# Performance work log

Hardware: AMD Instinct MI355X
Metric: run time of the kernel (lower is better)

Reference implementation:

```python
import jax, jax.numpy as jnp
import numpy as np

NHEAD = 8
STRIP = 7  # strip_width (horizontal strips, is_vertical=False)


def setup_inputs() -> dict:
    key = jax.random.key(0)
    k0, k1, k2 = jax.random.split(key, 3)
    B, H, W, C = 2, 112, 112, 256
    x = jax.random.normal(k0, (B, H * W, C), dtype=jnp.float32)
    # torch nn.Linear weights: (out_features, in_features)
    qkv_w = jax.random.normal(k1, (3 * C, C), dtype=jnp.float32) * 0.02
    proj_w = jax.random.normal(k2, (C, C), dtype=jnp.float32) * 0.02
    proj_b = jnp.zeros((C,), dtype=jnp.float32)
    return {"x": x, "qkv_w": qkv_w, "proj_w": proj_w, "proj_b": proj_b,
            "H_feat": 112, "W_feat": 112}


def reference(x, qkv_w, proj_w, proj_b, H_feat, W_feat):
    B, N, C = x.shape
    hd = C // NHEAD
    scale = hd ** -0.5
    n_strips = H_feat // STRIP
    L = STRIP * W_feat  # tokens per horizontal strip
    # window_partition with window (STRIP, W_feat): nwW==1, so a pure reshape
    xs = x.reshape(B * n_strips, L, C)
    # qkv projection (Linear: y = x @ W^T), then split q/k/v and heads
    qkv = jnp.einsum('bnc,dc->bnd', xs, qkv_w)
    qkv = qkv.reshape(B * n_strips, L, 3, NHEAD, hd)
    q, k, v = jnp.moveaxis(qkv, 2, 0)  # each (Bw, L, H, hd)
    attn = jnp.einsum('bnhd,bmhd->bhnm', q * scale, k)
    attn = jax.nn.softmax(attn, axis=-1)
    out = jnp.einsum('bhnm,bmhd->bnhd', attn, v).reshape(B * n_strips, L, C)
    out = jnp.einsum('bnc,dc->bnd', out, proj_w) + proj_b
    # window_reverse is again a pure reshape for horizontal strips
    return out.reshape(B, N, C)
```

## Files before the change

kernel.cpp:

```cpp
#include <hip/hip_runtime.h>
#include <hip/hip_bf16.h>

#define M_ROWS 25088
#define CDIM   256
#define QKVD   768
#define LWIN   784
#define NWINH  256

typedef __attribute__((ext_vector_type(8))) short short8v;
typedef __attribute__((ext_vector_type(4))) float floatx4;

#define CEQ 0.2550660106245232f

static __device__ __forceinline__ unsigned short f2bf(float f) {
    unsigned int x = __float_as_uint(f);
    x += 0x7fffu + ((x >> 16) & 1u);
    return (unsigned short)(x >> 16);
}
static __device__ __forceinline__ unsigned int cvt_pk_bf16(float a, float b) {
    unsigned int r;
    asm("v_cvt_pk_bf16_f32 %0, %1, %2" : "=v"(r) : "v"(a), "v"(b));
    return r;
}
static __device__ __forceinline__ void gld_lds16(const unsigned short* g,
                                                 unsigned short* l) {
    __builtin_amdgcn_global_load_lds(
        (const __attribute__((address_space(1))) unsigned int*)g,
        (__attribute__((address_space(3))) unsigned int*)l, 16, 0, 0);
}

#define N8_TOTAL ((M_ROWS * CDIM + QKVD * CDIM + CDIM * CDIM) / 8)

__global__ __launch_bounds__(256) void k_f2bf3(
    const float* __restrict__ s0,
    const float* __restrict__ s1,
    const float* __restrict__ s2,
    unsigned short* __restrict__ d0,
    unsigned short* __restrict__ d1,
    unsigned short* __restrict__ d2)
{
    const int n80 = (M_ROWS * CDIM) / 8;
    const int n81 = (QKVD * CDIM) / 8;
    for (int i = blockIdx.x * 256 + threadIdx.x; i < N8_TOTAL;
         i += gridDim.x * 256) {
        const float4* s4;
        uint4* d4;
        int j = i;
        if (j < n80)            { s4 = (const float4*)s0; d4 = (uint4*)d0; }
        else if ((j -= n80) < n81) { s4 = (const float4*)s1; d4 = (uint4*)d1; }
        else                    { j -= n81; s4 = (const float4*)s2; d4 = (uint4*)d2; }
        float4 a = s4[2 * j], b = s4[2 * j + 1];
        uint4 o;
        o.x = cvt_pk_bf16(a.x, a.y);
        o.y = cvt_pk_bf16(a.z, a.w);
        o.z = cvt_pk_bf16(b.x, b.y);
        o.w = cvt_pk_bf16(b.z, b.w);
        d4[j] = o;
    }
}

template <typename OUT_T, bool BIAS, bool SCALEQ>
__global__ __launch_bounds__(256, 2) void k_gemm_mfma(
    const unsigned short* __restrict__ A,
    const unsigned short* __restrict__ B,
    const float* __restrict__ bias,
    OUT_T* __restrict__ Y, int N)
{
    __shared__ __attribute__((aligned(16))) unsigned short As[128 * 64];
    __shared__ __attribute__((aligned(16))) unsigned short Bs[128 * 64];
    const int t = threadIdx.x;
    const int lane = t & 63, wv = t >> 6;
    const int lq = lane & 15, g = lane >> 4;
    const int wm = wv >> 1, wn = wv & 1;
    const int R0 = blockIdx.y * 128, C0 = blockIdx.x * 128;
    const int lrow = t >> 3, lch = (t & 7) * 8;

    floatx4 acc[4][4];
#pragma unroll
    for (int i = 0; i < 4; ++i)
#pragma unroll
        for (int j = 0; j < 4; ++j) acc[i][j] = (floatx4){0.f, 0.f, 0.f, 0.f};

    for (int kc = 0; kc < 256; kc += 64) {
#pragma unroll
        for (int i = 0; i < 4; ++i) {
            gld_lds16(A + (size_t)(R0 + i * 32 + lrow) * 256 + kc + lch,
                      As + (i * 32 + wv * 8) * 64);
            gld_lds16(B + (size_t)(C0 + i * 32 + lrow) * 256 + kc + lch,
                      Bs + (i * 32 + wv * 8) * 64);
        }
        __syncthreads();
#pragma unroll
        for (int kk = 0; kk < 64; kk += 32) {
            short8v af[4], bf[4];
#pragma unroll
            for (int mi = 0; mi < 4; ++mi)
                af[mi] = *(const short8v*)(As + (wm * 64 + mi * 16 + lq) * 64 +
                                           kk + g * 8);
#pragma unroll
            for (int ni = 0; ni < 4; ++ni)
                bf[ni] = *(const short8v*)(Bs + (wn * 64 + ni * 16 + lq) * 64 +
                                           kk + g * 8);
#pragma unroll
            for (int mi = 0; mi < 4; ++mi)
#pragma unroll
                for (int ni = 0; ni < 4; ++ni)
                    acc[mi][ni] = __builtin_amdgcn_mfma_f32_16x16x32_bf16(
                        af[mi], bf[ni], acc[mi][ni], 0, 0, 0);
        }
        __syncthreads();
    }

#pragma unroll
    for (int mi = 0; mi < 4; ++mi) {
        const size_t rb = (size_t)R0 + wm * 64 + mi * 16 + g * 4;
#pragma unroll
        for (int ni = 0; ni < 4; ++ni) {
            const int col = C0 + wn * 64 + ni * 16 + lq;
            float bv = 0.f;
            if constexpr (BIAS) bv = bias[col];
#pragma unroll
            for (int r = 0; r < 4; ++r) {
                float val = acc[mi][ni][r];
                if constexpr (SCALEQ) { if (col < 256) val *= CEQ; }
                val += bv;
                if constexpr (sizeof(OUT_T) == 2)
                    Y[(rb + r) * N + col] = (OUT_T)f2bf(val);
                else
                    Y[(rb + r) * N + col] = (OUT_T)val;
            }
        }
    }
}

#define KPITCH 36
#define VPITCH 404
#define KS_SZ  (LWIN * KPITCH)
#define ATTN_LDS (KS_SZ * 2 + 32 * VPITCH * 4)

__global__ __launch_bounds__(1024, 1) void k_attn_mfma(
    const unsigned short* __restrict__ qkv,
    unsigned short* __restrict__ ao)
{
    extern __shared__ unsigned short sm[];
    unsigned short* Ks = sm;
    unsigned int*   Vt = (unsigned int*)(sm + KS_SZ);
    const int t = threadIdx.x;
    const int lane = t & 63, wave = t >> 6;
    const int lq = lane & 15, g = lane >> 4;
    const int h = blockIdx.x & 7, w = blockIdx.x >> 3;
    const size_t rowbase = (size_t)w * LWIN;
    const unsigned short* base = qkv + rowbase * QKVD;

    for (int idx = t; idx < LWIN * 4; idx += 1024) {
        const int row = idx >> 2, c = idx & 3;
        uint4 kv = *(const uint4*)(base + (size_t)row * QKVD + 256 + h * 32 + c * 8);
        *(uint4*)(Ks + row * KPITCH + c * 8) = kv;
    }
    {
        const int c = t >> 8;
        const int p0 = t & 255;
        for (int tp = p0; tp < 392; tp += 256) {
            const int u = tp >> 4, tpp = tp & 15;
            const int a = tpp >> 3, gg = (tpp >> 1) & 3, rp = tpp & 1;
            const int wrd = u * 16 + gg * 4 + a * 2 + rp;
            union { uint4 u4; unsigned short s[8]; } x0, x1;
            x0.u4 = *(const uint4*)(base + (size_t)(2 * tp) * QKVD + 512 + h * 32 + c * 8);
            x1.u4 = *(const uint4*)(base + (size_t)(2 * tp + 1) * QKVD + 512 + h * 32 + c * 8);
#pragma unroll
            for (int j = 0; j < 8; ++j)
                Vt[(c * 8 + j) * VPITCH + wrd] =
                    (unsigned int)x0.s[j] | ((unsigned int)x1.s[j] << 16);
        }
    }
    for (int idx = t; idx < 32 * 8; idx += 1024) {
        const int d = idx >> 3, q = idx & 7;
        Vt[d * VPITCH + 384 + (q >> 1) * 4 + 2 + (q & 1)] = 0;
    }
    __syncthreads();

    const int ntile = (wave == 0) ? 4 : 3;
    const int tbase = (wave == 0) ? 0 : (3 * wave + 1);

    short8v qf[4];
#pragma unroll
    for (int n = 0; n < 4; ++n)
        if (n < ntile)
            qf[n] = *(const short8v*)(base +
                    (size_t)((tbase + n) * 16 + lq) * QKVD + h * 32 + g * 8);

    floatx4 oa[4][2];
#pragma unroll
    for (int n = 0; n < 4; ++n) {
        oa[n][0] = (floatx4){0.f, 0.f, 0.f, 0.f};
        oa[n][1] = (floatx4){0.f, 0.f, 0.f, 0.f};
    }
    float lsum[4] = {0.f, 0.f, 0.f, 0.f};

    for (int u = 0; u < 25; ++u) {
        unsigned int pw[4][4];
        __builtin_amdgcn_s_setprio(1);
        {
            short8v kf = *(const short8v*)(Ks + (size_t)(2 * u * 16 + lq) * KPITCH + g * 8);
#pragma unroll
            for (int n = 0; n < 4; ++n) if (n < ntile) {
                floatx4 st = __builtin_amdgcn_mfma_f32_16x16x32_bf16(
                    kf, qf[n], (floatx4){0.f, 0.f, 0.f, 0.f}, 0, 0, 0);
                float p0 = __builtin_amdgcn_exp2f(st[0]);
                float p1 = __builtin_amdgcn_exp2f(st[1]);
                float p2 = __builtin_amdgcn_exp2f(st[2]);
                float p3 = __builtin_amdgcn_exp2f(st[3]);
                lsum[n] += (p0 + p1) + (p2 + p3);
                pw[n][0] = cvt_pk_bf16(p0, p1);
                pw[n][1] = cvt_pk_bf16(p2, p3);
            }
        }
        if (u < 24) {
            short8v kf = *(const short8v*)(Ks + (size_t)((2 * u + 1) * 16 + lq) * KPITCH + g * 8);
#pragma unroll
            for (int n = 0; n < 4; ++n) if (n < ntile) {
                floatx4 st = __builtin_amdgcn_mfma_f32_16x16x32_bf16(
                    kf, qf[n], (floatx4){0.f, 0.f, 0.f, 0.f}, 0, 0, 0);
                float p0 = __builtin_amdgcn_exp2f(st[0]);
                float p1 = __builtin_amdgcn_exp2f(st[1]);
                float p2 = __builtin_amdgcn_exp2f(st[2]);
                float p3 = __builtin_amdgcn_exp2f(st[3]);
                lsum[n] += (p0 + p1) + (p2 + p3);
                pw[n][2] = cvt_pk_bf16(p0, p1);
                pw[n][3] = cvt_pk_bf16(p2, p3);
            }
        } else {
#pragma unroll
            for (int n = 0; n < 4; ++n) if (n < ntile) {
                pw[n][2] = 0u; pw[n][3] = 0u;
            }
        }
        const unsigned short* vrow0 = (const unsigned short*)Vt;
        short8v v0 = *(const short8v*)(vrow0 + (size_t)lq * (VPITCH * 2) + u * 32 + g * 8);
        short8v v1 = *(const short8v*)(vrow0 + (size_t)(lq + 16) * (VPITCH * 2) + u * 32 + g * 8);
#pragma unroll
        for (int n = 0; n < 4; ++n) if (n < ntile) {
            union { unsigned int wd[4]; short8v v; } pu;
            pu.wd[0] = pw[n][0]; pu.wd[1] = pw[n][1];
            pu.wd[2] = pw[n][2]; pu.wd[3] = pw[n][3];
            oa[n][0] = __builtin_amdgcn_mfma_f32_16x16x32_bf16(pu.v, v0, oa[n][0], 0, 0, 0);
            oa[n][1] = __builtin_amdgcn_mfma_f32_16x16x32_bf16(pu.v, v1, oa[n][1], 0, 0, 0);
        }
        __builtin_amdgcn_s_setprio(0);
    }

#pragma unroll
    for (int n = 0; n < 4; ++n) if (n < ntile) {
        float l = lsum[n];
        l += __shfl_xor(l, 16);
        l += __shfl_xor(l, 32);
        float inv = 1.f / l;
        const size_t orow0 = rowbase + (size_t)(tbase + n) * 16;
#pragma unroll
        for (int r = 0; r < 4; ++r) {
            float ir = __shfl(inv, (lane & 48) | (g * 4 + r));
            size_t ob = (orow0 + g * 4 + r) * CDIM + h * 32;
            ao[ob + lq]      = f2bf(oa[n][0][r] * ir);
            ao[ob + 16 + lq] = f2bf(oa[n][1][r] * ir);
        }
    }
}

extern "C" void kernel_launch(void* const* d_in, const int* in_sizes, int n_in,
                              void* d_out, int out_size, void* d_ws, size_t ws_size,
                              hipStream_t stream) {
    const float* x      = (const float*)d_in[0];
    const float* qkv_w  = (const float*)d_in[1];
    const float* proj_w = (const float*)d_in[2];
    const float* proj_b = (const float*)d_in[3];
    float* out = (float*)d_out;

    unsigned short* qkvb = (unsigned short*)d_ws;
    unsigned short* xb   = qkvb + (size_t)M_ROWS * QKVD;
    unsigned short* aob  = xb;
    unsigned short* wqb  = xb + (size_t)M_ROWS * CDIM;
    unsigned short* wpb  = wqb + (size_t)QKVD * CDIM;

    hipFuncSetAttribute((const void*)k_attn_mfma,
                        hipFuncAttributeMaxDynamicSharedMemorySize, ATTN_LDS);

    k_f2bf3<<<2048, 256, 0, stream>>>(x, qkv_w, proj_w, xb, wqb, wpb);

    k_gemm_mfma<unsigned short, false, true>
        <<<dim3(QKVD / 128, M_ROWS / 128), 256, 0, stream>>>(
            xb, wqb, nullptr, qkvb, QKVD);

    k_attn_mfma<<<dim3(NWINH), 1024, ATTN_LDS, stream>>>(qkvb, aob);

    k_gemm_mfma<float, true, false>
        <<<dim3(CDIM / 128, M_ROWS / 128), 256, 0, stream>>>(
            aob, wpb, proj_b, out, CDIM);
}
```

Measured before the change: 83.80 us.

## Split the leftover 49th query tile across all waves using key-range partial sums

Each window has 49 query tiles of 16 rows for 16 waves. Before, wave 0 handled 4 tiles and the others 3, so one wave set the critical path. Now every wave handles 3 tiles, and the 49th tile is split by key range across all 16 waves. Each wave writes its partial output and softmax sum to LDS, and wave 0 reduces them after a barrier. This balances the MFMA work but adds LDS space, a block-wide sync and a serial reduction tail in wave 0. The do48 condition inside the loop may also cost registers or branching.

```diff
diff --git a/kernel.cpp b/kernel.cpp
--- a/kernel.cpp
+++ b/kernel.cpp
@@ -136,7 +136,10 @@
 #define KPITCH 36
 #define VPITCH 404
 #define KS_SZ  (LWIN * KPITCH)
-#define ATTN_LDS (KS_SZ * 2 + 32 * VPITCH * 4)
+#define VT_SH  (32 * VPITCH * 2)
+#define PART_OFF (KS_SZ + VT_SH)
+#define PART_BYTES (16 * 64 * 12 * 4)
+#define ATTN_LDS (PART_OFF * 2 + PART_BYTES)
 
 __global__ __launch_bounds__(1024, 1) void k_attn_mfma(
     const unsigned short* __restrict__ qkv,
@@ -145,6 +148,7 @@
     extern __shared__ unsigned short sm[];
     unsigned short* Ks = sm;
     unsigned int*   Vt = (unsigned int*)(sm + KS_SZ);
+    float*          pb = (float*)(sm + PART_OFF);
     const int t = threadIdx.x;
     const int lane = t & 63, wave = t >> 6;
     const int lq = lane & 15, g = lane >> 4;
@@ -179,15 +183,16 @@
     }
     __syncthreads();
 
-    const int ntile = (wave == 0) ? 4 : 3;
-    const int tbase = (wave == 0) ? 0 : (3 * wave + 1);
+    const int myu0 = (wave < 9) ? 2 * wave : wave + 9;
+    const int myu1 = (wave < 9) ? 2 * wave + 2 : wave + 10;
 
     short8v qf[4];
 #pragma unroll
-    for (int n = 0; n < 4; ++n)
-        if (n < ntile)
-            qf[n] = *(const short8v*)(base +
-                    (size_t)((tbase + n) * 16 + lq) * QKVD + h * 32 + g * 8);
+    for (int n = 0; n < 3; ++n)
+        qf[n] = *(const short8v*)(base +
+                (size_t)((wave + n * 16) * 16 + lq) * QKVD + h * 32 + g * 8);
+    qf[3] = *(const short8v*)(base +
+            (size_t)(48 * 16 + lq) * QKVD + h * 32 + g * 8);
 
     floatx4 oa[4][2];
 #pragma unroll
@@ -198,12 +203,13 @@
     float lsum[4] = {0.f, 0.f, 0.f, 0.f};
 
     for (int u = 0; u < 25; ++u) {
+        const bool do48 = (u >= myu0) && (u < myu1);
         unsigned int pw[4][4];
         __builtin_amdgcn_s_setprio(1);
         {
             short8v kf = *(const short8v*)(Ks + (size_t)(2 * u * 16 + lq) * KPITCH + g * 8);
 #pragma unroll
-            for (int n = 0; n < 4; ++n) if (n < ntile) {
+            for (int n = 0; n < 4; ++n) if (n < 3 || do48) {
                 floatx4 st = __builtin_amdgcn_mfma_f32_16x16x32_bf16(
                     kf, qf[n], (floatx4){0.f, 0.f, 0.f, 0.f}, 0, 0, 0);
                 float p0 = __builtin_amdgcn_exp2f(st[0]);
@@ -218,7 +224,7 @@
         if (u < 24) {
             short8v kf = *(const short8v*)(Ks + (size_t)((2 * u + 1) * 16 + lq) * KPITCH + g * 8);
 #pragma unroll
-            for (int n = 0; n < 4; ++n) if (n < ntile) {
+            for (int n = 0; n < 4; ++n) if (n < 3 || do48) {
                 floatx4 st = __builtin_amdgcn_mfma_f32_16x16x32_bf16(
                     kf, qf[n], (floatx4){0.f, 0.f, 0.f, 0.f}, 0, 0, 0);
                 float p0 = __builtin_amdgcn_exp2f(st[0]);
@@ -231,7 +237,7 @@
             }
         } else {
 #pragma unroll
-            for (int n = 0; n < 4; ++n) if (n < ntile) {
+            for (int n = 0; n < 4; ++n) if (n < 3 || do48) {
                 pw[n][2] = 0u; pw[n][3] = 0u;
             }
         }
@@ -239,7 +245,7 @@
         short8v v0 = *(const short8v*)(vrow0 + (size_t)lq * (VPITCH * 2) + u * 32 + g * 8);
         short8v v1 = *(const short8v*)(vrow0 + (size_t)(lq + 16) * (VPITCH * 2) + u * 32 + g * 8);
 #pragma unroll
-        for (int n = 0; n < 4; ++n) if (n < ntile) {
+        for (int n = 0; n < 4; ++n) if (n < 3 || do48) {
             union { unsigned int wd[4]; short8v v; } pu;
             pu.wd[0] = pw[n][0]; pu.wd[1] = pw[n][1];
             pu.wd[2] = pw[n][2]; pu.wd[3] = pw[n][3];
@@ -250,18 +256,51 @@
     }
 
 #pragma unroll
-    for (int n = 0; n < 4; ++n) if (n < ntile) {
+    for (int n = 0; n < 3; ++n) {
         float l = lsum[n];
         l += __shfl_xor(l, 16);
         l += __shfl_xor(l, 32);
         float inv = 1.f / l;
-        const size_t orow0 = rowbase + (size_t)(tbase + n) * 16;
+        const size_t orow0 = rowbase + (size_t)(wave + n * 16) * 16;
 #pragma unroll
         for (int r = 0; r < 4; ++r) {
             float ir = __shfl(inv, (lane & 48) | (g * 4 + r));
             size_t ob = (orow0 + g * 4 + r) * CDIM + h * 32;
             ao[ob + lq]      = f2bf(oa[n][0][r] * ir);
             ao[ob + 16 + lq] = f2bf(oa[n][1][r] * ir);
+        }
+    }
+
+    {
+        float* mypb = pb + (wave * 64 + lane) * 12;
+#pragma unroll
+        for (int r = 0; r < 4; ++r) {
+            mypb[r]     = oa[3][0][r];
+            mypb[4 + r] = oa[3][1][r];
+        }
+        mypb[8] = lsum[3];
+    }
+    __syncthreads();
+    if (wave == 0) {
+        floatx4 s0 = {0.f, 0.f, 0.f, 0.f}, s1 = {0.f, 0.f, 0.f, 0.f};
+        float sl = 0.f;
+        for (int v2 = 0; v2 < 16; ++v2) {
+            const float* q = pb + (v2 * 64 + lane) * 12;
+            floatx4 a0 = *(const floatx4*)q;
+            floatx4 a1 = *(const floatx4*)(q + 4);
+            s0 += a0; s1 += a1;
+            sl += q[8];
+        }
+        sl += __shfl_xor(sl, 16);
+        sl += __shfl_xor(sl, 32);
+        float inv = 1.f / sl;
+        const size_t orow0 = rowbase + 768;
+#pragma unroll
+        for (int r = 0; r < 4; ++r) {
+            float ir = __shfl(inv, (lane & 48) | (g * 4 + r));
+            size_t ob = (orow0 + g * 4 + r) * CDIM + h * 32;
+            ao[ob + lq]      = f2bf(s0[r] * ir);
+            ao[ob + 16 + lq] = f2bf(s1[r] * ir);
         }
     }
 }
```

Result: no change. 84.62 us (+1.0%).

## Stream K/V chunks through double-buffered LDS and split query tiles across blocks

Applied to the files above, without the earlier changes.

The attention kernel changes from one 1024-thread block per window-head, which loads the whole K and transposed V into LDS, to seven 512-thread blocks per window-head. Each wave owns a single 16-row query tile, and K/V arrive in 64-row chunks through a double-buffered LDS stage that overlaps with compute. The aim is to shrink the per-block LDS footprint, raise occupancy and hide the global-load latency of the up-front staging. In exchange, every block re-reads the full K/V for its window-head, giving roughly seven times the L2 traffic. Each K fragment is reused by only one query tile instead of three or four, the loop adds a barrier per chunk, and the last block of each window-head leaves 7 of its 8 waves idle.

```diff
diff --git a/kernel.cpp b/kernel.cpp
--- a/kernel.cpp
+++ b/kernel.cpp
@@ -133,135 +133,149 @@
     }
 }
 
-#define KPITCH 36
-#define VPITCH 404
-#define KS_SZ  (LWIN * KPITCH)
-#define ATTN_LDS (KS_SZ * 2 + 32 * VPITCH * 4)
-
-__global__ __launch_bounds__(1024, 1) void k_attn_mfma(
+#define C_KP 36
+#define C_VP 36
+#define KC_SH (64 * C_KP)
+#define VC_W  (32 * C_VP)
+#define ATTN_LDS (2 * KC_SH * 2 + 2 * VC_W * 4)
+
+__global__ __launch_bounds__(512, 6) void k_attn_stream(
     const unsigned short* __restrict__ qkv,
     unsigned short* __restrict__ ao)
 {
     extern __shared__ unsigned short sm[];
-    unsigned short* Ks = sm;
-    unsigned int*   Vt = (unsigned int*)(sm + KS_SZ);
+    unsigned short* Kc = sm;
+    unsigned int*   Vc = (unsigned int*)(sm + 2 * KC_SH);
     const int t = threadIdx.x;
     const int lane = t & 63, wave = t >> 6;
     const int lq = lane & 15, g = lane >> 4;
-    const int h = blockIdx.x & 7, w = blockIdx.x >> 3;
+    const int wh = blockIdx.x & 255, b = blockIdx.x >> 8;
+    const int h = wh & 7, w = wh >> 3;
     const size_t rowbase = (size_t)w * LWIN;
     const unsigned short* base = qkv + rowbase * QKVD;
-
-    for (int idx = t; idx < LWIN * 4; idx += 1024) {
-        const int row = idx >> 2, c = idx & 3;
-        uint4 kv = *(const uint4*)(base + (size_t)row * QKVD + 256 + h * 32 + c * 8);
-        *(uint4*)(Ks + row * KPITCH + c * 8) = kv;
-    }
-    {
-        const int c = t >> 8;
-        const int p0 = t & 255;
-        for (int tp = p0; tp < 392; tp += 256) {
-            const int u = tp >> 4, tpp = tp & 15;
-            const int a = tpp >> 3, gg = (tpp >> 1) & 3, rp = tpp & 1;
-            const int wrd = u * 16 + gg * 4 + a * 2 + rp;
-            union { uint4 u4; unsigned short s[8]; } x0, x1;
-            x0.u4 = *(const uint4*)(base + (size_t)(2 * tp) * QKVD + 512 + h * 32 + c * 8);
-            x1.u4 = *(const uint4*)(base + (size_t)(2 * tp + 1) * QKVD + 512 + h * 32 + c * 8);
-#pragma unroll
-            for (int j = 0; j < 8; ++j)
-                Vt[(c * 8 + j) * VPITCH + wrd] =
-                    (unsigned int)x0.s[j] | ((unsigned int)x1.s[j] << 16);
-        }
-    }
-    for (int idx = t; idx < 32 * 8; idx += 1024) {
-        const int d = idx >> 3, q = idx & 7;
-        Vt[d * VPITCH + 384 + (q >> 1) * 4 + 2 + (q & 1)] = 0;
-    }
+    const int tile = b * 8 + wave;
+    const bool have = (tile < 49);
+
+    short8v qf = {0, 0, 0, 0, 0, 0, 0, 0};
+    if (have)
+        qf = *(const short8v*)(base + (size_t)(tile * 16 + lq) * QKVD +
+                               h * 32 + g * 8);
+
+    floatx4 oa0 = {0.f, 0.f, 0.f, 0.f}, oa1 = {0.f, 0.f, 0.f, 0.f};
+    float lsum = 0.f;
+
+    auto stage = [&](int c) {
+        unsigned short* Kb = Kc + (c & 1) * KC_SH;
+        unsigned int*   Vb = Vc + (c & 1) * VC_W;
+        if (t < 256) {
+            const int row = t >> 2, cc = t & 3;
+            const int grow = c * 64 + row;
+            if (grow < LWIN) {
+                uint4 kv = *(const uint4*)(base + (size_t)grow * QKVD +
+                                           256 + h * 32 + cc * 8);
+                *(uint4*)(Kb + row * C_KP + cc * 8) = kv;
+            }
+        } else if (t < 384) {
+            const int i2 = t - 256;
+            const int tpl = i2 >> 2, cc = i2 & 3;
+            const int tp = c * 32 + tpl;
+            if (tp < 392) {
+                const int u = tp >> 4, up = u - 2 * c, tpp = tp & 15;
+                const int a = tpp >> 3, gg = (tpp >> 1) & 3, rp = tpp & 1;
+                const int wrd = up * 16 + gg * 4 + a * 2 + rp;
+                union { uint4 u4; unsigned short s[8]; } x0, x1;
+                x0.u4 = *(const uint4*)(base + (size_t)(2 * tp) * QKVD +
+                                        512 + h * 32 + cc * 8);
+                x1.u4 = *(const uint4*)(base + (size_t)(2 * tp + 1) * QKVD +
+                                        512 + h * 32 + cc * 8);
+#pragma unroll
+                for (int j = 0; j < 8; ++j)
+                    Vb[(cc * 8 + j) * C_VP + wrd] =
+                        (unsigned int)x0.s[j] | ((unsigned int)x1.s[j] << 16);
+            }
+        } else {
+            if (c == 12) {
+                const int i3 = t - 384;
+                const int d = i3 >> 2, q2 = i3 & 3;
+                unsigned int* vb = Vb + d * C_VP;
+                vb[q2 * 4 + 2] = 0u;
+                vb[q2 * 4 + 3] = 0u;
+            }
+        }
+    };
+
+    auto compute = [&](int c) {
+        const unsigned short* Kb = Kc + (c & 1) * KC_SH;
+        const unsigned short* Vb16 =
+            (const unsigned short*)(Vc + (c & 1) * VC_W);
+        __builtin_amdgcn_s_setprio(1);
+#pragma unroll
+        for (int up = 0; up < 2; ++up) {
+            const int u = 2 * c + up;
+            if (u < 25) {
+                unsigned int pw0, pw1, pw2, pw3;
+                {
+                    short8v kf = *(const short8v*)(
+                        Kb + (size_t)((2 * up) * 16 + lq) * C_KP + g * 8);
+                    floatx4 st = __builtin_amdgcn_mfma_f32_16x16x32_bf16(
+                        kf, qf, (floatx4){0.f, 0.f, 0.f, 0.f}, 0, 0, 0);
+                    float p0 = __builtin_amdgcn_exp2f(st[0]);
+                    float p1 = __builtin_amdgcn_exp2f(st[1]);
+                    float p2 = __builtin_amdgcn_exp2f(st[2]);
+                    float p3 = __builtin_amdgcn_exp2f(st[3]);
+                    lsum += (p0 + p1) + (p2 + p3);
+                    pw0 = cvt_pk_bf16(p0, p1);
+                    pw1 = cvt_pk_bf16(p2, p3);
+                }
+                if (u < 24) {
+                    short8v kf = *(const short8v*)(
+                        Kb + (size_t)((2 * up + 1) * 16 + lq) * C_KP + g * 8);
+                    floatx4 st = __builtin_amdgcn_mfma_f32_16x16x32_bf16(
+                        kf, qf, (floatx4){0.f, 0.f, 0.f, 0.f}, 0, 0, 0);
+                    float p0 = __builtin_amdgcn_exp2f(st[0]);
+                    float p1 = __builtin_amdgcn_exp2f(st[1]);
+                    float p2 = __builtin_amdgcn_exp2f(st[2]);
+                    float p3 = __builtin_amdgcn_exp2f(st[3]);
+                    lsum += (p0 + p1) + (p2 + p3);
+                    pw2 = cvt_pk_bf16(p0, p1);
+                    pw3 = cvt_pk_bf16(p2, p3);
+                } else {
+                    pw2 = 0u; pw3 = 0u;
+                }
+                const int vo = up * 32 + g * 8;
+                short8v v0 = *(const short8v*)(
+                    Vb16 + (size_t)lq * (C_VP * 2) + vo);
+                short8v v1 = *(const short8v*)(
+                    Vb16 + (size_t)(lq + 16) * (C_VP * 2) + vo);
+                union { unsigned int wd[4]; short8v v; } pu;
+                pu.wd[0] = pw0; pu.wd[1] = pw1; pu.wd[2] = pw2; pu.wd[3] = pw3;
+                oa0 = __builtin_amdgcn_mfma_f32_16x16x32_bf16(pu.v, v0, oa0, 0, 0, 0);
+                oa1 = __builtin_amdgcn_mfma_f32_16x16x32_bf16(pu.v, v1, oa1, 0, 0, 0);
+            }
+        }
+        __builtin_amdgcn_s_setprio(0);
+    };
+
+    stage(0);
     __syncthreads();
-
-    const int ntile = (wave == 0) ? 4 : 3;
-    const int tbase = (wave == 0) ? 0 : (3 * wave + 1);
-
-    short8v qf[4];
-#pragma unroll
-    for (int n = 0; n < 4; ++n)
-        if (n < ntile)
-            qf[n] = *(const short8v*)(base +
-                    (size_t)((tbase + n) * 16 + lq) * QKVD + h * 32 + g * 8);
-
-    floatx4 oa[4][2];
-#pragma unroll
-    for (int n = 0; n < 4; ++n) {
-        oa[n][0] = (floatx4){0.f, 0.f, 0.f, 0.f};
-        oa[n][1] = (floatx4){0.f, 0.f, 0.f, 0.f};
-    }
-    float lsum[4] = {0.f, 0.f, 0.f, 0.f};
-
-    for (int u = 0; u < 25; ++u) {
-        unsigned int pw[4][4];
-        __builtin_amdgcn_s_setprio(1);
-        {
-            short8v kf = *(const short8v*)(Ks + (size_t)(2 * u * 16 + lq) * KPITCH + g * 8);
-#pragma unroll
-            for (int n = 0; n < 4; ++n) if (n < ntile) {
-                floatx4 st = __builtin_amdgcn_mfma_f32_16x16x32_bf16(
-                    kf, qf[n], (floatx4){0.f, 0.f, 0.f, 0.f}, 0, 0, 0);
-                float p0 = __builtin_amdgcn_exp2f(st[0]);
-                float p1 = __builtin_amdgcn_exp2f(st[1]);
-                float p2 = __builtin_amdgcn_exp2f(st[2]);
-                float p3 = __builtin_amdgcn_exp2f(st[3]);
-                lsum[n] += (p0 + p1) + (p2 + p3);
-                pw[n][0] = cvt_pk_bf16(p0, p1);
-                pw[n][1] = cvt_pk_bf16(p2, p3);
-            }
-        }
-        if (u < 24) {
-            short8v kf = *(const short8v*)(Ks + (size_t)((2 * u + 1) * 16 + lq) * KPITCH + g * 8);
-#pragma unroll
-            for (int n = 0; n < 4; ++n) if (n < ntile) {
-                floatx4 st = __builtin_amdgcn_mfma_f32_16x16x32_bf16(
-                    kf, qf[n], (floatx4){0.f, 0.f, 0.f, 0.f}, 0, 0, 0);
-                float p0 = __builtin_amdgcn_exp2f(st[0]);
-                float p1 = __builtin_amdgcn_exp2f(st[1]);
-                float p2 = __builtin_amdgcn_exp2f(st[2]);
-                float p3 = __builtin_amdgcn_exp2f(st[3]);
-                lsum[n] += (p0 + p1) + (p2 + p3);
-                pw[n][2] = cvt_pk_bf16(p0, p1);
-                pw[n][3] = cvt_pk_bf16(p2, p3);
-            }
-        } else {
-#pragma unroll
-            for (int n = 0; n < 4; ++n) if (n < ntile) {
-                pw[n][2] = 0u; pw[n][3] = 0u;
-            }
-        }
-        const unsigned short* vrow0 = (const unsigned short*)Vt;
-        short8v v0 = *(const short8v*)(vrow0 + (size_t)lq * (VPITCH * 2) + u * 32 + g * 8);
-        short8v v1 = *(const short8v*)(vrow0 + (size_t)(lq + 16) * (VPITCH * 2) + u * 32 + g * 8);
-#pragma unroll
-        for (int n = 0; n < 4; ++n) if (n < ntile) {
-            union { unsigned int wd[4]; short8v v; } pu;
-            pu.wd[0] = pw[n][0]; pu.wd[1] = pw[n][1];
-            pu.wd[2] = pw[n][2]; pu.wd[3] = pw[n][3];
-            oa[n][0] = __builtin_amdgcn_mfma_f32_16x16x32_bf16(pu.v, v0, oa[n][0], 0, 0, 0);
-            oa[n][1] = __builtin_amdgcn_mfma_f32_16x16x32_bf16(pu.v, v1, oa[n][1], 0, 0, 0);
-        }
-        __builtin_amdgcn_s_setprio(0);
-    }
-
-#pragma unroll
-    for (int n = 0; n < 4; ++n) if (n < ntile) {
-        float l = lsum[n];
+    for (int c = 0; c < 13; ++c) {
+        if (c < 12) stage(c + 1);
+        if (have) compute(c);
+        __syncthreads();
+    }
+
+    if (have) {
+        float l = lsum;
         l += __shfl_xor(l, 16);
         l += __shfl_xor(l, 32);
         float inv = 1.f / l;
-        const size_t orow0 = rowbase + (size_t)(tbase + n) * 16;
+        const size_t orow0 = rowbase + (size_t)tile * 16;
 #pragma unroll
         for (int r = 0; r < 4; ++r) {
             float ir = __shfl(inv, (lane & 48) | (g * 4 + r));
             size_t ob = (orow0 + g * 4 + r) * CDIM + h * 32;
-            ao[ob + lq]      = f2bf(oa[n][0][r] * ir);
-            ao[ob + 16 + lq] = f2bf(oa[n][1][r] * ir);
+            ao[ob + lq]      = f2bf(oa0[r] * ir);
+            ao[ob + 16 + lq] = f2bf(oa1[r] * ir);
         }
     }
 }
@@ -281,7 +295,7 @@
     unsigned short* wqb  = xb + (size_t)M_ROWS * CDIM;
     unsigned short* wpb  = wqb + (size_t)QKVD * CDIM;
 
-    hipFuncSetAttribute((const void*)k_attn_mfma,
+    hipFuncSetAttribute((const void*)k_attn_stream,
                         hipFuncAttributeMaxDynamicSharedMemorySize, ATTN_LDS);
 
     k_f2bf3<<<2048, 256, 0, stream>>>(x, qkv_w, proj_w, xb, wqb, wpb);
@@ -290,7 +304,7 @@
         <<<dim3(QKVD / 128, M_ROWS / 128), 256, 0, stream>>>(
             xb, wqb, nullptr, qkvb, QKVD);
 
-    k_attn_mfma<<<dim3(NWINH), 1024, ATTN_LDS, stream>>>(qkvb, aob);
+    k_attn_stream<<<dim3(7 * NWINH), 512, ATTN_LDS, stream>>>(qkvb, aob);
 
     k_gemm_mfma<float, true, false>
         <<<dim3(CDIM / 128, M_ROWS / 128), 256, 0, stream>>>(
```

After: 144.5 us. +72.4%, slower.
